# Kernel optimization log

Hardware: AMD Instinct MI355X
Metric: run time of the kernel (lower is better)

## Reference

```python
import jax, jax.numpy as jnp
import numpy as np
from jax import lax

RHO = 0.1          # init kwarg rho
CG_ITERS = 15      # dc_torch(..., 0.001, 15): fixed 15 CG iterations
EPS = 1e-12


def _c(x):  # (..., 2) real pair -> complex
    return lax.complex(x[..., 0], x[..., 1])


def _r(x):  # complex -> (..., 2) real pair
    return jnp.stack([jnp.real(x), jnp.imag(x)], axis=-1)


def fft2c(x):
    ax = (-2, -1)
    return jnp.fft.fftshift(jnp.fft.fft2(jnp.fft.ifftshift(x, axes=ax), axes=ax, norm='ortho'), axes=ax)


def ifft2c(x):
    ax = (-2, -1)
    return jnp.fft.fftshift(jnp.fft.ifft2(jnp.fft.ifftshift(x, axes=ax), axes=ax, norm='ortho'), axes=ax)


def setup_inputs() -> dict:
    key = jax.random.key(0)
    k0, k1, k2, k3 = jax.random.split(key, 4)
    B, S, C, H, W = 1, 4, 16, 320, 320
    K = jax.random.normal(k0, (B, S, C, H, W, 2), jnp.float32)
    I = jax.random.normal(k1, (B, S, H, W, 2), jnp.float32)
    csm = jax.random.normal(k2, (B, C, H, W, 2), jnp.float32) * 0.2
    mask = (jax.random.uniform(k3, (B, S, H, W)) < 0.35).astype(jnp.float32)
    return {'K_mulShot_sigCoil': K, 'I': I, 'csm': csm, 'mask': mask}


def _dc_cg(kdata, img, s, m):
    # kdata: [B,S,C,H,W] complex, img: [B,S,H,W], s: [B,C,H,W], m: [B,S,H,W]
    def E(x):                      # image [B,S,H,W] -> k-space [B,S,C,H,W]
        return m[:, :, None] * fft2c(s[:, None] * x[:, :, None])

    def EH(y):                     # adjoint: coil-combine
        return jnp.sum(jnp.conj(s)[:, None] * ifft2c(m[:, :, None] * y), axis=2)

    def AtA(x):
        return EH(E(x)) + RHO * x

    rhs = EH(kdata) + RHO * img
    x0 = jnp.zeros_like(rhs)
    r0 = rhs
    rs0 = jnp.real(jnp.vdot(r0, r0))

    def body(carry, _):
        x, r, p, rs = carry
        Ap = AtA(p)
        alpha = rs / (jnp.real(jnp.vdot(p, Ap)) + EPS)
        x = x + alpha * p
        r = r - alpha * Ap
        rs_new = jnp.real(jnp.vdot(r, r))
        p = r + (rs_new / (rs + EPS)) * p
        return (x, r, p, rs_new), None

    (x, _, _, _), _ = lax.scan(body, (x0, r0, r0, rs0), None, length=CG_ITERS)
    return x


def reference(K_mulShot_sigCoil, I, csm, mask):
    kdata = _c(K_mulShot_sigCoil)
    img = _c(I)
    s = _c(csm)
    x = _dc_cg(kdata, img, s, mask)   # image-domain CG solution
    K = fft2c(x)                      # sf.dc_torch returns k-space
    out = ifft2c(K)                   # layer returns I = ifft2c(K)
    return _r(out)
```

## Files before the change

### kernel.cpp

```cpp
#include <hip/hip_runtime.h>
#include <math.h>


#define NDIM 320
#define HHALF 160
#define HW (NDIM*NDIM)
#define NS 4
#define NC 16
#define RHO_ 0.1f
#define CG_ITERS 15

typedef float v2f __attribute__((ext_vector_type(2)));

__device__ __forceinline__ void wsync(){
    __builtin_amdgcn_fence(__ATOMIC_ACQ_REL, "wavefront");
    __builtin_amdgcn_wave_barrier();
}

__device__ __forceinline__ float wred(float v){
    #pragma unroll
    for (int o=32;o>0;o>>=1) v += __shfl_down(v,o,64);
    return v;
}

__device__ __forceinline__ v2f cmulf(v2f a, v2f b){
    return (v2f){a.x,a.x}*b + (v2f){-a.y,a.y}*(v2f){b.y,b.x};
}

template<int SIGMA>
__device__ __forceinline__ v2f cmulw(v2f a, v2f w){
    v2f wb = (SIGMA<0) ? w : (v2f){w.x, -w.y};
    return cmulf(a, wb);
}

template<int SIGMA>
__device__ __forceinline__ v2f mulj(v2f z){
    return (v2f){ -(float)SIGMA*z.y, (float)SIGMA*z.x };
}

template<int SIGMA>
__device__ __forceinline__ void radix5(const v2f* u, v2f* v){
    const float C1 = 0.30901699437494742f, S1 = 0.95105651629515357f;
    const float C2 = -0.80901699437494745f, S2 = 0.58778525229247312f;
    v2f t1=u[1]+u[4], t2=u[2]+u[3], t3=u[1]-u[4], t4=u[2]-u[3];
    v[0] = u[0] + t1 + t2;
    v2f m1 = u[0] + t1*C1 + t2*C2;
    v2f m2 = u[0] + t1*C2 + t2*C1;
    v2f n1 = t3*S1 + t4*S2;
    v2f n2 = t3*S2 - t4*S1;
    v2f j1 = mulj<SIGMA>(n1), j2 = mulj<SIGMA>(n2);
    v[1]=m1+j1; v[4]=m1-j1; v[2]=m2+j2; v[3]=m2-j2;
}

template<int SIGMA>
__device__ __forceinline__ void dft8(const v2f* u, v2f* y){
    const float C = 0.70710678118654752f;
    v2f a0=u[0]+u[4], a1=u[0]-u[4];
    v2f a2=u[2]+u[6], a3=u[2]-u[6];
    v2f a4=u[1]+u[5], a5=u[1]-u[5];
    v2f a6=u[3]+u[7], a7=u[3]-u[7];
    v2f j3 = mulj<SIGMA>(a3);
    v2f E0=a0+a2, E2=a0-a2;
    v2f E1=a1+j3, E3=a1-j3;
    v2f j7 = mulj<SIGMA>(a7);
    v2f O0=a4+a6, O2=a4-a6;
    v2f O1=a5+j7, O3=a5-j7;
    v2f W1 = (O1 + mulj<SIGMA>(O1)) * C;
    v2f jO2 = mulj<SIGMA>(O2);
    v2f W3 = (mulj<SIGMA>(O3) - O3) * C;
    y[0]=E0+O0; y[4]=E0-O0;
    y[1]=E1+W1; y[5]=E1-W1;
    y[2]=E2+jO2; y[6]=E2-jO2;
    y[3]=E3+W3; y[7]=E3-W3;
}

template<int SIGMA>
__device__ __forceinline__ void s1_from_regs(v2f* __restrict__ A, int t,
                                             const v2f* u5){
    v2f v[5];
    radix5<SIGMA>(u5, v);
    #pragma unroll
    for (int c=0;c<5;++c) A[5*t + c] = v[c];
}

template<int SIGMA>
__device__ __forceinline__ void s1_stage(v2f* __restrict__ A, int t){
    v2f u[5];
    #pragma unroll
    for (int q=0;q<5;++q) u[q] = A[t + 64*q];
    wsync();
    s1_from_regs<SIGMA>(A, t, u);
}

template<int SIGMA>
__device__ __forceinline__ void s2_stage(v2f* __restrict__ A, int t, v2f w40){
    if (t < 40){
        v2f u[8];
        #pragma unroll
        for (int q=0;q<8;++q) u[q] = A[t + 40*q];
        wsync();
        v2f wc = w40;
        u[1] = cmulw<SIGMA>(u[1], wc);
        #pragma unroll
        for (int q=2;q<8;++q){ wc = cmulf(wc, w40); u[q] = cmulw<SIGMA>(u[q], wc); }
        v2f v[8];
        dft8<SIGMA>(u, v);
        int k = t % 5, jb = t / 5;
        int base = jb*40 + k;
        #pragma unroll
        for (int c=0;c<8;++c) A[base + 5*c] = v[c];
    }
}

template<int SIGMA>
__device__ __forceinline__ void s3_toregs(const v2f* __restrict__ A, int t,
                                          v2f w320, v2f* v){
    if (t < 40){
        v2f u[8];
        #pragma unroll
        for (int q=0;q<8;++q) u[q] = A[t + 40*q];
        v2f wc = w320;
        u[1] = cmulw<SIGMA>(u[1], wc);
        #pragma unroll
        for (int q=2;q<8;++q){ wc = cmulf(wc, w320); u[q] = cmulw<SIGMA>(u[q], wc); }
        dft8<SIGMA>(u, v);
    }
}

template<int SIGMA>
__device__ __forceinline__ void a3_fromregs(v2f* __restrict__ A, int t,
                                            v2f w320, const v2f* vin){
    if (t < 40){
        v2f u[8];
        dft8<SIGMA>(vin, u);
        v2f wc = w320;
        u[1] = cmulw<SIGMA>(u[1], wc);
        #pragma unroll
        for (int q=2;q<8;++q){ wc = cmulf(wc, w320); u[q] = cmulw<SIGMA>(u[q], wc); }
        #pragma unroll
        for (int q=0;q<8;++q) A[t + 40*q] = u[q];
    }
}

template<int SIGMA>
__device__ __forceinline__ void a2_stage(v2f* __restrict__ A, int t, v2f w40){
    if (t < 40){
        int k = t % 5, jb = t / 5;
        int base = jb*40 + k;
        v2f v[8];
        #pragma unroll
        for (int c=0;c<8;++c) v[c] = A[base + 5*c];
        wsync();
        v2f u[8];
        dft8<SIGMA>(v, u);
        v2f wc = w40;
        u[1] = cmulw<SIGMA>(u[1], wc);
        #pragma unroll
        for (int q=2;q<8;++q){ wc = cmulf(wc, w40); u[q] = cmulw<SIGMA>(u[q], wc); }
        #pragma unroll
        for (int q=0;q<8;++q) A[t + 40*q] = u[q];
    }
}

template<int SIGMA>
__device__ __forceinline__ void a1_toregs(const v2f* __restrict__ A, int t,
                                          v2f* out5){
    v2f v[5];
    #pragma unroll
    for (int c=0;c<5;++c) v[c] = A[5*t + c];
    radix5<SIGMA>(v, out5);
}

__device__ __forceinline__ void make_w(int t, v2f& w40, v2f& w320){
    float sn, cs;
    const float n2pi = -6.283185307179586f;
    __sincosf(n2pi*(float)(t%5)/40.f, &sn, &cs); w40  = (v2f){cs, sn};
    __sincosf(n2pi*(float)t/320.f,    &sn, &cs); w320 = (v2f){cs, sn};
}

__device__ __forceinline__ int sh160(int i){ return i < HHALF ? i + HHALF : i - HHALF; }

__global__ void k_prep(const v2f* __restrict__ kin, const float* __restrict__ mask,
                       const v2f* __restrict__ csm, v2f* __restrict__ sP,
                       float* __restrict__ mscT, v2f* __restrict__ K,
                       float* __restrict__ scal)
{
    int gid = blockIdx.x*blockDim.x + threadIdx.x;
    int gsz = gridDim.x*blockDim.x;
    if (gid < 64) scal[gid] = 0.f;
    for (int i = gid; i < NC*HW; i += gsz){
        int w = i % NDIM; int h = (i/NDIM) % NDIM; int c = i/HW;
        sP[i] = csm[(c*NDIM + sh160(h))*NDIM + sh160(w)];
    }
    for (int i = gid; i < NS*HW; i += gsz){
        int h = i % NDIM; int wc = (i/NDIM)%NDIM; int s = i/HW;
        float m = mask[(s*NDIM + sh160(h))*NDIM + sh160(wc)];
        mscT[i] = m*m*(1.0f/102400.0f);
    }
    for (int i = gid; i < NS*NC*HW; i += gsz){
        int w = i % NDIM; int h = (i/NDIM)%NDIM; int sc = i/HW;
        int s = sc >> 4;
        int hs = sh160(h), ws = sh160(w);
        float m = mask[(s*NDIM + hs)*NDIM + ws];
        v2f kv = kin[((long)sc*NDIM + hs)*NDIM + ws];
        float f = m*(1.0f/320.0f);
        K[i] = kv * f;
    }
}

__global__ __launch_bounds__(256) void k_passA(
    const v2f* __restrict__ rv_, const v2f* __restrict__ pOld,
    v2f* __restrict__ pNew, const v2f* __restrict__ sP,
    v2f* __restrict__ K, float* __restrict__ scal, int iter)
{
    int bid = blockIdx.x;
    int cg = bid & 3;
    int hg = (bid>>2) % 80;
    int s  = bid / (4*80);
    int tid = threadIdx.x; int rl = tid>>6; int t = tid&63;
    int h = hg*4 + rl;
    __shared__ v2f bufA[4][NDIM];
    v2f* A = &bufA[rl][0];
    v2f w40, w320; make_w(t, w40, w320);
    float beta = 0.f;
    if (iter > 0) beta = scal[iter] / (scal[iter-1] + 1e-12f);
    long base = (long)s*HW + h*NDIM;
    v2f pv[5];
    #pragma unroll
    for (int j=0;j<5;++j){
        int idx = t + 64*j;
        v2f rr = rv_[base+idx];
        if (iter > 0){
            v2f pp = pOld[base+idx];
            pv[j] = rr + pp*beta;
        } else pv[j] = rr;
    }
    if (cg == 0){
        float d = 0.f;
        #pragma unroll
        for (int j=0;j<5;++j){
            pNew[base + t + 64*j] = pv[j];
            d += pv[j].x*pv[j].x + pv[j].y*pv[j].y;
        }
        float wd = wred(d);
        if (t==0) atomicAdd(&scal[16+iter], RHO_*wd);
    }
    int c = cg*4;
    const v2f* srow = sP + (long)c*HW + h*NDIM;
    v2f sv[5];
    #pragma unroll
    for (int j=0;j<5;++j) sv[j] = srow[t+64*j];
    #pragma unroll
    for (int c0=0;c0<4;++c0){
        v2f u5[5];
        #pragma unroll
        for (int j=0;j<5;++j) u5[j] = cmulf(sv[j], pv[j]);
        v2f sv2[5];
        if (c0<3){
            const v2f* sr2 = srow + (long)(c0+1)*HW;
            #pragma unroll
            for (int j=0;j<5;++j) sv2[j] = sr2[t+64*j];
        }
        wsync();
        s1_from_regs<-1>(A, t, u5);
        wsync();
        s2_stage<-1>(A, t, w40);
        wsync();
        v2f v8[8];
        s3_toregs<-1>(A, t, w320, v8);
        long kb = ((long)(s*NC + c + c0))*HW + h*NDIM;
        if (t < 40){
            #pragma unroll
            for (int cc=0;cc<8;++cc) K[kb + t + 40*cc] = v8[cc];
        }
        if (c0<3){
            #pragma unroll
            for (int j=0;j<5;++j) sv[j]=sv2[j];
        }
    }
}

__global__ __launch_bounds__(512) void k_passB(v2f* __restrict__ K,
    const float* __restrict__ mscT, int doMask)
{
    constexpr int L = 324;
    int bid = blockIdx.x;
    int wt = bid % 40;
    int sc = bid / 40;
    int s = sc >> 4;
    int tid = threadIdx.x;
    int col = tid >> 6;
    int t = tid & 63;
    int w0 = wt*8;
    __shared__ v2f bufA[8][L];
    v2f w40, w320; make_w(t, w40, w320);
    float mv[8];
    if (doMask && t < 40){
        const float* mcol = mscT + (long)s*HW + (long)(w0+col)*NDIM;
        #pragma unroll
        for (int cc=0;cc<8;++cc) mv[cc] = mcol[t+40*cc];
    }
    long gb = (long)sc*HW;
    int wl = tid & 7, hb = tid >> 3;
    #pragma unroll
    for (int j=0;j<5;++j){
        int hh = hb + 64*j;
        bufA[wl][hh] = K[gb + (long)hh*NDIM + w0 + wl];
    }
    __syncthreads();
    v2f* A = &bufA[col][0];
    if (doMask){
        s1_stage<-1>(A, t);
        wsync();
        s2_stage<-1>(A, t, w40);
        wsync();
        v2f v8[8];
        s3_toregs<-1>(A, t, w320, v8);
        if (t < 40){
            #pragma unroll
            for (int cc=0;cc<8;++cc) v8[cc] = v8[cc]*mv[cc];
        }
        wsync();
        a3_fromregs<1>(A, t, w320, v8);
        wsync();
        a2_stage<1>(A, t, w40);
        wsync();
        v2f x5[5];
        a1_toregs<1>(A, t, x5);
        wsync();
        #pragma unroll
        for (int q=0;q<5;++q) A[t + 64*q] = x5[q];
    } else {
        s1_stage<1>(A, t);
        wsync();
        s2_stage<1>(A, t, w40);
        wsync();
        v2f v8[8];
        s3_toregs<1>(A, t, w320, v8);
        wsync();
        if (t < 40){
            #pragma unroll
            for (int cc=0;cc<8;++cc) A[t + 40*cc] = v8[cc];
        }
    }
    __syncthreads();
    #pragma unroll
    for (int j=0;j<5;++j){
        int hh = hb + 64*j;
        K[gb + (long)hh*NDIM + w0 + wl] = bufA[wl][hh];
    }
}

__global__ __launch_bounds__(256) void k_passC2(
    const v2f* __restrict__ K, const v2f* __restrict__ sP,
    const v2f* __restrict__ pVec, v2f* __restrict__ part,
    float* __restrict__ scal, int dotSlot, int doDot)
{
    int bid = blockIdx.x;
    int cg = bid & 3;
    int hg = (bid>>2) % 80;
    int s  = bid / (4*80);
    int tid = threadIdx.x; int rl = tid>>6; int t = tid&63;
    int h = hg*4 + rl;
    __shared__ v2f bufA[4][NDIM];
    __shared__ float redS[4];
    v2f* A = &bufA[rl][0];
    v2f w40, w320; make_w(t, w40, w320);
    int c = cg*4;
    long kb0 = ((long)(s*NC + c))*HW + h*NDIM;
    const v2f* srow = sP + (long)c*HW + h*NDIM;
    v2f kv[8], sv[5];
    if (t < 40){
        #pragma unroll
        for (int cc=0;cc<8;++cc) kv[cc] = K[kb0 + t + 40*cc];
    }
    #pragma unroll
    for (int j=0;j<5;++j) sv[j] = srow[t+64*j];
    v2f acc[5];
    #pragma unroll
    for (int j=0;j<5;++j) acc[j]=(v2f){0.f,0.f};
    #pragma unroll
    for (int c0=0;c0<4;++c0){
        a3_fromregs<1>(A, t, w320, kv);
        v2f kv2[8], sv2[5];
        if (c0<3){
            long kb = kb0 + (long)(c0+1)*HW;
            const v2f* sr2 = srow + (long)(c0+1)*HW;
            if (t < 40){
                #pragma unroll
                for (int cc=0;cc<8;++cc) kv2[cc] = K[kb + t + 40*cc];
            }
            #pragma unroll
            for (int j=0;j<5;++j) sv2[j] = sr2[t+64*j];
        }
        wsync();
        a2_stage<1>(A, t, w40);
        wsync();
        v2f x5[5];
        a1_toregs<1>(A, t, x5);
        #pragma unroll
        for (int j=0;j<5;++j){
            acc[j] += (v2f){sv[j].x,sv[j].x}*x5[j]
                    + (v2f){sv[j].y,-sv[j].y}*(v2f){x5[j].y,x5[j].x};
        }
        wsync();
        if (c0<3){
            #pragma unroll
            for (int cc=0;cc<8;++cc) kv[cc]=kv2[cc];
            #pragma unroll
            for (int j=0;j<5;++j) sv[j]=sv2[j];
        }
    }
    long pbase = (long)s*HW + h*NDIM;
    long obase = ((long)cg*NS + s)*HW + h*NDIM;
    float dot = 0.f;
    #pragma unroll
    for (int j=0;j<5;++j){
        int idx=t+64*j;
        part[obase+idx] = acc[j];
        if (doDot){
            v2f pp = pVec[pbase+idx];
            dot += pp.x*acc[j].x + pp.y*acc[j].y;
        }
    }
    if (doDot){
        float wd = wred(dot);
        if (t==0) redS[rl] = wd;
        __syncthreads();
        if (tid==0) atomicAdd(&scal[dotSlot], redS[0]+redS[1]+redS[2]+redS[3]);
    }
}

__global__ __launch_bounds__(256) void k_rhs_fin(
    const v2f* __restrict__ part, const v2f* __restrict__ Iin,
    v2f* __restrict__ r, v2f* __restrict__ x, float* __restrict__ scal)
{
    __shared__ float red[256];
    int gid = blockIdx.x*blockDim.x + threadIdx.x;
    int gsz = gridDim.x*blockDim.x;
    float rs = 0.f;
    const int NV = NS*HW;
    for (int i = gid; i < NV; i += gsz){
        int w = i % NDIM; int h = (i/NDIM)%NDIM; int s = i/HW;
        v2f iv = Iin[((long)s*NDIM + sh160(h))*NDIM + sh160(w)];
        v2f rr = part[i] + part[NV+i] + part[2*NV+i] + part[3*NV+i] + iv*RHO_;
        r[i] = rr;
        x[i] = (v2f){0.f,0.f};
        rs += rr.x*rr.x + rr.y*rr.y;
    }
    red[threadIdx.x]=rs; __syncthreads();
    for (int o=128;o>0;o>>=1){ if (threadIdx.x<o) red[threadIdx.x]+=red[threadIdx.x+o]; __syncthreads(); }
    if (threadIdx.x==0) atomicAdd(&scal[0], red[0]);
}

__global__ __launch_bounds__(256) void k_update(
    v2f* __restrict__ x, v2f* __restrict__ r,
    const v2f* __restrict__ p, const v2f* __restrict__ part,
    float* __restrict__ scal, int iter)
{
    __shared__ float red[256];
    float alpha = scal[iter] / (scal[16+iter] + 1e-12f);
    int gid = blockIdx.x*blockDim.x + threadIdx.x;
    int gsz = gridDim.x*blockDim.x;
    float rs = 0.f;
    const int NV = NS*HW;
    for (int i = gid; i < NV; i += gsz){
        v2f pvv=p[i];
        v2f av = part[i] + part[NV+i] + part[2*NV+i] + part[3*NV+i] + pvv*RHO_;
        v2f xv = x[i] + pvv*alpha;
        v2f rv = r[i] - av*alpha;
        x[i]=xv; r[i]=rv;
        rs += rv.x*rv.x + rv.y*rv.y;
    }
    red[threadIdx.x]=rs; __syncthreads();
    for (int o=128;o>0;o>>=1){ if (threadIdx.x<o) red[threadIdx.x]+=red[threadIdx.x+o]; __syncthreads(); }
    if (threadIdx.x==0) atomicAdd(&scal[iter+1], red[0]);
}

__global__ void k_final(const v2f* __restrict__ x, v2f* __restrict__ out)
{
    int gid = blockIdx.x*blockDim.x + threadIdx.x;
    int gsz = gridDim.x*blockDim.x;
    for (int i = gid; i < NS*HW; i += gsz){
        int w = i % NDIM; int h = (i/NDIM)%NDIM; int s = i/HW;
        out[i] = x[(long)s*HW + sh160(h)*NDIM + sh160(w)];
    }
}

extern "C" void kernel_launch(void* const* d_in, const int* in_sizes, int n_in,
                              void* d_out, int out_size, void* d_ws, size_t ws_size,
                              hipStream_t stream) {
    (void)in_sizes; (void)n_in; (void)out_size; (void)ws_size;
    const v2f* kin  = (const v2f*)d_in[0];
    const v2f* Iin  = (const v2f*)d_in[1];
    const v2f* csm  = (const v2f*)d_in[2];
    const float* mask = (const float*)d_in[3];

    char* w = (char*)d_ws;
    size_t off = 0;
    float* scal = (float*)(w+off);  off += 1024;
    v2f* sP   = (v2f*)(w+off); off += (size_t)NC*HW*8;
    float* mscT = (float*)(w+off); off += (size_t)NS*HW*4;
    v2f* K    = (v2f*)(w+off); off += (size_t)NS*NC*HW*8;
    v2f* x    = (v2f*)(w+off); off += (size_t)NS*HW*8;
    v2f* r    = (v2f*)(w+off); off += (size_t)NS*HW*8;
    v2f* pA   = (v2f*)(w+off); off += (size_t)NS*HW*8;
    v2f* pB   = (v2f*)(w+off); off += (size_t)NS*HW*8;
    v2f* part = (v2f*)(w+off); off += (size_t)4*NS*HW*8;

    k_prep<<<2048,256,0,stream>>>(kin, mask, csm, sP, mscT, K, scal);
    k_passB<<<NS*NC*40,512,0,stream>>>(K, mscT, 0);
    k_passC2<<<NS*80*4,256,0,stream>>>(K, sP, r, part, scal, 63, 0);
    k_rhs_fin<<<640,256,0,stream>>>(part, Iin, r, x, scal);

    for (int it=0; it<CG_ITERS; ++it){
        v2f* pNew = (it&1)? pB : pA;
        v2f* pOld = (it&1)? pA : pB;
        k_passA<<<NS*80*4,256,0,stream>>>(r, pOld, pNew, sP, K, scal, it);
        k_passB<<<NS*NC*40,512,0,stream>>>(K, mscT, 1);
        k_passC2<<<NS*80*4,256,0,stream>>>(K, sP, pNew, part, scal, 16+it, 1);
        k_update<<<640,256,0,stream>>>(x, r, pNew, part, scal, it);
    }
    k_final<<<512,256,0,stream>>>(x, (v2f*)d_out);
}
```

Before: 1.617 ms.

## Process two FFT rows/columns per wavefront to raise per-thread ILP

Each 64-lane wavefront now computes two independent 320-point FFTs at once (paired radix-5/radix-8 stages) instead of one, in the row-forward, column, and adjoint-row kernels. The column kernel drops from 512 to 256 threads per block with the same eight columns per block, and the other kernels double shared memory per wave. The intent is to amortize twiddle generation, wave syncs and per-FFT overhead and to expose more instruction-level parallelism, at the cost of higher register pressure and fewer waves per block.

```diff
diff --git a/kernel.cpp b/kernel.cpp
--- a/kernel.cpp
+++ b/kernel.cpp
@@ -75,100 +75,123 @@
 }
 
 template<int SIGMA>
-__device__ __forceinline__ void s1_from_regs(v2f* __restrict__ A, int t,
-                                             const v2f* u5){
-    v2f v[5];
-    radix5<SIGMA>(u5, v);
-    #pragma unroll
-    for (int c=0;c<5;++c) A[5*t + c] = v[c];
-}
-
-template<int SIGMA>
-__device__ __forceinline__ void s1_stage(v2f* __restrict__ A, int t){
-    v2f u[5];
-    #pragma unroll
-    for (int q=0;q<5;++q) u[q] = A[t + 64*q];
+__device__ __forceinline__ void s1_write_pair(v2f* __restrict__ A0,
+                                              v2f* __restrict__ A1, int t,
+                                              const v2f* u0, const v2f* u1){
+    v2f v0[5], v1[5];
+    radix5<SIGMA>(u0, v0);
+    radix5<SIGMA>(u1, v1);
+    #pragma unroll
+    for (int c=0;c<5;++c){ A0[5*t+c]=v0[c]; A1[5*t+c]=v1[c]; }
+}
+
+template<int SIGMA>
+__device__ __forceinline__ void s1_pair(v2f* __restrict__ A0,
+                                        v2f* __restrict__ A1, int t){
+    v2f u0[5], u1[5];
+    #pragma unroll
+    for (int q=0;q<5;++q){ u0[q]=A0[t+64*q]; u1[q]=A1[t+64*q]; }
     wsync();
-    s1_from_regs<SIGMA>(A, t, u);
-}
-
-template<int SIGMA>
-__device__ __forceinline__ void s2_stage(v2f* __restrict__ A, int t, v2f w40){
+    s1_write_pair<SIGMA>(A0,A1,t,u0,u1);
+}
+
+template<int SIGMA>
+__device__ __forceinline__ void tw_dft8_pair(v2f* u0, v2f* u1, v2f w,
+                                             v2f* v0, v2f* v1){
+    v2f wc = w;
+    u0[1]=cmulw<SIGMA>(u0[1],wc); u1[1]=cmulw<SIGMA>(u1[1],wc);
+    #pragma unroll
+    for (int q=2;q<8;++q){
+        wc = cmulf(wc, w);
+        u0[q]=cmulw<SIGMA>(u0[q],wc); u1[q]=cmulw<SIGMA>(u1[q],wc);
+    }
+    dft8<SIGMA>(u0, v0);
+    dft8<SIGMA>(u1, v1);
+}
+
+template<int SIGMA>
+__device__ __forceinline__ void s2_pair(v2f* __restrict__ A0,
+                                        v2f* __restrict__ A1, int t, v2f w40){
     if (t < 40){
-        v2f u[8];
-        #pragma unroll
-        for (int q=0;q<8;++q) u[q] = A[t + 40*q];
-        wsync();
-        v2f wc = w40;
-        u[1] = cmulw<SIGMA>(u[1], wc);
-        #pragma unroll
-        for (int q=2;q<8;++q){ wc = cmulf(wc, w40); u[q] = cmulw<SIGMA>(u[q], wc); }
-        v2f v[8];
-        dft8<SIGMA>(u, v);
+        v2f u0[8], u1[8];
+        #pragma unroll
+        for (int q=0;q<8;++q){ u0[q]=A0[t+40*q]; u1[q]=A1[t+40*q]; }
+        wsync();
+        v2f v0[8], v1[8];
+        tw_dft8_pair<SIGMA>(u0,u1,w40,v0,v1);
         int k = t % 5, jb = t / 5;
         int base = jb*40 + k;
         #pragma unroll
-        for (int c=0;c<8;++c) A[base + 5*c] = v[c];
-    }
-}
-
-template<int SIGMA>
-__device__ __forceinline__ void s3_toregs(const v2f* __restrict__ A, int t,
-                                          v2f w320, v2f* v){
+        for (int c=0;c<8;++c){ A0[base+5*c]=v0[c]; A1[base+5*c]=v1[c]; }
+    }
+}
+
+template<int SIGMA>
+__device__ __forceinline__ void s3_pair(const v2f* __restrict__ A0,
+                                        const v2f* __restrict__ A1, int t,
+                                        v2f w320, v2f* v0, v2f* v1){
     if (t < 40){
-        v2f u[8];
-        #pragma unroll
-        for (int q=0;q<8;++q) u[q] = A[t + 40*q];
+        v2f u0[8], u1[8];
+        #pragma unroll
+        for (int q=0;q<8;++q){ u0[q]=A0[t+40*q]; u1[q]=A1[t+40*q]; }
+        tw_dft8_pair<SIGMA>(u0,u1,w320,v0,v1);
+    }
+}
+
+template<int SIGMA>
+__device__ __forceinline__ void a3_pair(v2f* __restrict__ A0,
+                                        v2f* __restrict__ A1, int t,
+                                        v2f w320, const v2f* i0, const v2f* i1){
+    if (t < 40){
+        v2f u0[8], u1[8];
+        dft8<SIGMA>(i0, u0);
+        dft8<SIGMA>(i1, u1);
         v2f wc = w320;
-        u[1] = cmulw<SIGMA>(u[1], wc);
-        #pragma unroll
-        for (int q=2;q<8;++q){ wc = cmulf(wc, w320); u[q] = cmulw<SIGMA>(u[q], wc); }
-        dft8<SIGMA>(u, v);
-    }
-}
-
-template<int SIGMA>
-__device__ __forceinline__ void a3_fromregs(v2f* __restrict__ A, int t,
-                                            v2f w320, const v2f* vin){
-    if (t < 40){
-        v2f u[8];
-        dft8<SIGMA>(vin, u);
-        v2f wc = w320;
-        u[1] = cmulw<SIGMA>(u[1], wc);
-        #pragma unroll
-        for (int q=2;q<8;++q){ wc = cmulf(wc, w320); u[q] = cmulw<SIGMA>(u[q], wc); }
-        #pragma unroll
-        for (int q=0;q<8;++q) A[t + 40*q] = u[q];
-    }
-}
-
-template<int SIGMA>
-__device__ __forceinline__ void a2_stage(v2f* __restrict__ A, int t, v2f w40){
+        u0[1]=cmulw<SIGMA>(u0[1],wc); u1[1]=cmulw<SIGMA>(u1[1],wc);
+        #pragma unroll
+        for (int q=2;q<8;++q){
+            wc = cmulf(wc, w320);
+            u0[q]=cmulw<SIGMA>(u0[q],wc); u1[q]=cmulw<SIGMA>(u1[q],wc);
+        }
+        #pragma unroll
+        for (int q=0;q<8;++q){ A0[t+40*q]=u0[q]; A1[t+40*q]=u1[q]; }
+    }
+}
+
+template<int SIGMA>
+__device__ __forceinline__ void a2_pair(v2f* __restrict__ A0,
+                                        v2f* __restrict__ A1, int t, v2f w40){
     if (t < 40){
         int k = t % 5, jb = t / 5;
         int base = jb*40 + k;
-        v2f v[8];
-        #pragma unroll
-        for (int c=0;c<8;++c) v[c] = A[base + 5*c];
-        wsync();
-        v2f u[8];
-        dft8<SIGMA>(v, u);
+        v2f v0[8], v1[8];
+        #pragma unroll
+        for (int c=0;c<8;++c){ v0[c]=A0[base+5*c]; v1[c]=A1[base+5*c]; }
+        wsync();
+        v2f u0[8], u1[8];
+        dft8<SIGMA>(v0, u0);
+        dft8<SIGMA>(v1, u1);
         v2f wc = w40;
-        u[1] = cmulw<SIGMA>(u[1], wc);
-        #pragma unroll
-        for (int q=2;q<8;++q){ wc = cmulf(wc, w40); u[q] = cmulw<SIGMA>(u[q], wc); }
-        #pragma unroll
-        for (int q=0;q<8;++q) A[t + 40*q] = u[q];
-    }
-}
-
-template<int SIGMA>
-__device__ __forceinline__ void a1_toregs(const v2f* __restrict__ A, int t,
-                                          v2f* out5){
-    v2f v[5];
-    #pragma unroll
-    for (int c=0;c<5;++c) v[c] = A[5*t + c];
-    radix5<SIGMA>(v, out5);
+        u0[1]=cmulw<SIGMA>(u0[1],wc); u1[1]=cmulw<SIGMA>(u1[1],wc);
+        #pragma unroll
+        for (int q=2;q<8;++q){
+            wc = cmulf(wc, w40);
+            u0[q]=cmulw<SIGMA>(u0[q],wc); u1[q]=cmulw<SIGMA>(u1[q],wc);
+        }
+        #pragma unroll
+        for (int q=0;q<8;++q){ A0[t+40*q]=u0[q]; A1[t+40*q]=u1[q]; }
+    }
+}
+
+template<int SIGMA>
+__device__ __forceinline__ void a1_pair(const v2f* __restrict__ A0,
+                                        const v2f* __restrict__ A1, int t,
+                                        v2f* o0, v2f* o1){
+    v2f v0[5], v1[5];
+    #pragma unroll
+    for (int c=0;c<5;++c){ v0[c]=A0[5*t+c]; v1[c]=A1[5*t+c]; }
+    radix5<SIGMA>(v0, o0);
+    radix5<SIGMA>(v1, o1);
 }
 
 __device__ __forceinline__ void make_w(int t, v2f& w40, v2f& w320){
@@ -219,8 +242,9 @@
     int s  = bid / (4*80);
     int tid = threadIdx.x; int rl = tid>>6; int t = tid&63;
     int h = hg*4 + rl;
-    __shared__ v2f bufA[4][NDIM];
-    v2f* A = &bufA[rl][0];
+    __shared__ v2f buf[8][NDIM];
+    v2f* A0 = &buf[2*rl][0];
+    v2f* A1 = &buf[2*rl+1][0];
     v2f w40, w320; make_w(t, w40, w320);
     float beta = 0.f;
     if (iter > 0) beta = scal[iter] / (scal[iter-1] + 1e-12f);
@@ -247,40 +271,43 @@
     }
     int c = cg*4;
     const v2f* srow = sP + (long)c*HW + h*NDIM;
-    v2f sv[5];
-    #pragma unroll
-    for (int j=0;j<5;++j) sv[j] = srow[t+64*j];
-    #pragma unroll
-    for (int c0=0;c0<4;++c0){
-        v2f u5[5];
-        #pragma unroll
-        for (int j=0;j<5;++j) u5[j] = cmulf(sv[j], pv[j]);
-        v2f sv2[5];
-        if (c0<3){
-            const v2f* sr2 = srow + (long)(c0+1)*HW;
-            #pragma unroll
-            for (int j=0;j<5;++j) sv2[j] = sr2[t+64*j];
-        }
-        wsync();
-        s1_from_regs<-1>(A, t, u5);
-        wsync();
-        s2_stage<-1>(A, t, w40);
-        wsync();
-        v2f v8[8];
-        s3_toregs<-1>(A, t, w320, v8);
-        long kb = ((long)(s*NC + c + c0))*HW + h*NDIM;
+    v2f sv0[5], sv1[5];
+    #pragma unroll
+    for (int j=0;j<5;++j){ sv0[j] = srow[t+64*j]; sv1[j] = srow[HW + t+64*j]; }
+    #pragma unroll
+    for (int pair=0;pair<2;++pair){
+        v2f u0[5], u1[5];
+        #pragma unroll
+        for (int j=0;j<5;++j){ u0[j]=cmulf(sv0[j],pv[j]); u1[j]=cmulf(sv1[j],pv[j]); }
+        v2f sn0[5], sn1[5];
+        if (pair==0){
+            const v2f* sr2 = srow + (long)2*HW;
+            #pragma unroll
+            for (int j=0;j<5;++j){ sn0[j]=sr2[t+64*j]; sn1[j]=sr2[HW + t+64*j]; }
+        }
+        wsync();
+        s1_write_pair<-1>(A0,A1,t,u0,u1);
+        wsync();
+        s2_pair<-1>(A0,A1,t,w40);
+        wsync();
+        v2f v0[8], v1[8];
+        s3_pair<-1>(A0,A1,t,w320,v0,v1);
+        long kb = ((long)(s*NC + c + 2*pair))*HW + h*NDIM;
         if (t < 40){
             #pragma unroll
-            for (int cc=0;cc<8;++cc) K[kb + t + 40*cc] = v8[cc];
-        }
-        if (c0<3){
-            #pragma unroll
-            for (int j=0;j<5;++j) sv[j]=sv2[j];
-        }
-    }
-}
-
-__global__ __launch_bounds__(512) void k_passB(v2f* __restrict__ K,
+            for (int cc=0;cc<8;++cc){
+                K[kb + t + 40*cc]      = v0[cc];
+                K[kb + HW + t + 40*cc] = v1[cc];
+            }
+        }
+        if (pair==0){
+            #pragma unroll
+            for (int j=0;j<5;++j){ sv0[j]=sn0[j]; sv1[j]=sn1[j]; }
+        }
+    }
+}
+
+__global__ __launch_bounds__(256) void k_passB(v2f* __restrict__ K,
     const float* __restrict__ mscT, int doMask)
 {
     constexpr int L = 324;
@@ -292,62 +319,63 @@
     int col = tid >> 6;
     int t = tid & 63;
     int w0 = wt*8;
-    __shared__ v2f bufA[8][L];
+    __shared__ v2f buf[8][L];
+    v2f* A0 = &buf[2*col][0];
+    v2f* A1 = &buf[2*col+1][0];
     v2f w40, w320; make_w(t, w40, w320);
-    float mv[8];
+    float mv0[8], mv1[8];
     if (doMask && t < 40){
-        const float* mcol = mscT + (long)s*HW + (long)(w0+col)*NDIM;
-        #pragma unroll
-        for (int cc=0;cc<8;++cc) mv[cc] = mcol[t+40*cc];
+        const float* mcol = mscT + (long)s*HW + (long)(w0+2*col)*NDIM;
+        #pragma unroll
+        for (int cc=0;cc<8;++cc){ mv0[cc]=mcol[t+40*cc]; mv1[cc]=mcol[NDIM + t+40*cc]; }
     }
     long gb = (long)sc*HW;
     int wl = tid & 7, hb = tid >> 3;
     #pragma unroll
-    for (int j=0;j<5;++j){
-        int hh = hb + 64*j;
-        bufA[wl][hh] = K[gb + (long)hh*NDIM + w0 + wl];
+    for (int j=0;j<10;++j){
+        int hh = hb + 32*j;
+        buf[wl][hh] = K[gb + (long)hh*NDIM + w0 + wl];
     }
     __syncthreads();
-    v2f* A = &bufA[col][0];
     if (doMask){
-        s1_stage<-1>(A, t);
-        wsync();
-        s2_stage<-1>(A, t, w40);
-        wsync();
-        v2f v8[8];
-        s3_toregs<-1>(A, t, w320, v8);
+        s1_pair<-1>(A0,A1,t);
+        wsync();
+        s2_pair<-1>(A0,A1,t,w40);
+        wsync();
+        v2f v0[8], v1[8];
+        s3_pair<-1>(A0,A1,t,w320,v0,v1);
         if (t < 40){
             #pragma unroll
-            for (int cc=0;cc<8;++cc) v8[cc] = v8[cc]*mv[cc];
-        }
-        wsync();
-        a3_fromregs<1>(A, t, w320, v8);
-        wsync();
-        a2_stage<1>(A, t, w40);
-        wsync();
-        v2f x5[5];
-        a1_toregs<1>(A, t, x5);
-        wsync();
-        #pragma unroll
-        for (int q=0;q<5;++q) A[t + 64*q] = x5[q];
+            for (int cc=0;cc<8;++cc){ v0[cc]=v0[cc]*mv0[cc]; v1[cc]=v1[cc]*mv1[cc]; }
+        }
+        wsync();
+        a3_pair<1>(A0,A1,t,w320,v0,v1);
+        wsync();
+        a2_pair<1>(A0,A1,t,w40);
+        wsync();
+        v2f x0[5], x1[5];
+        a1_pair<1>(A0,A1,t,x0,x1);
+        wsync();
+        #pragma unroll
+        for (int q=0;q<5;++q){ A0[t+64*q]=x0[q]; A1[t+64*q]=x1[q]; }
     } else {
-        s1_stage<1>(A, t);
-        wsync();
-        s2_stage<1>(A, t, w40);
-        wsync();
-        v2f v8[8];
-        s3_toregs<1>(A, t, w320, v8);
+        s1_pair<1>(A0,A1,t);
+        wsync();
+        s2_pair<1>(A0,A1,t,w40);
+        wsync();
+        v2f v0[8], v1[8];
+        s3_pair<1>(A0,A1,t,w320,v0,v1);
         wsync();
         if (t < 40){
             #pragma unroll
-            for (int cc=0;cc<8;++cc) A[t + 40*cc] = v8[cc];
+            for (int cc=0;cc<8;++cc){ A0[t+40*cc]=v0[cc]; A1[t+40*cc]=v1[cc]; }
         }
     }
     __syncthreads();
     #pragma unroll
-    for (int j=0;j<5;++j){
-        int hh = hb + 64*j;
-        K[gb + (long)hh*NDIM + w0 + wl] = bufA[wl][hh];
+    for (int j=0;j<10;++j){
+        int hh = hb + 32*j;
+        K[gb + (long)hh*NDIM + w0 + wl] = buf[wl][hh];
     }
 }
 
@@ -362,53 +390,56 @@
     int s  = bid / (4*80);
     int tid = threadIdx.x; int rl = tid>>6; int t = tid&63;
     int h = hg*4 + rl;
-    __shared__ v2f bufA[4][NDIM];
+    __shared__ v2f buf[8][NDIM];
     __shared__ float redS[4];
-    v2f* A = &bufA[rl][0];
+    v2f* A0 = &buf[2*rl][0];
+    v2f* A1 = &buf[2*rl+1][0];
     v2f w40, w320; make_w(t, w40, w320);
     int c = cg*4;
     long kb0 = ((long)(s*NC + c))*HW + h*NDIM;
     const v2f* srow = sP + (long)c*HW + h*NDIM;
-    v2f kv[8], sv[5];
+    v2f kv0[8], kv1[8], sv0[5], sv1[5];
     if (t < 40){
         #pragma unroll
-        for (int cc=0;cc<8;++cc) kv[cc] = K[kb0 + t + 40*cc];
-    }
-    #pragma unroll
-    for (int j=0;j<5;++j) sv[j] = srow[t+64*j];
+        for (int cc=0;cc<8;++cc){ kv0[cc]=K[kb0 + t+40*cc]; kv1[cc]=K[kb0 + HW + t+40*cc]; }
+    }
+    #pragma unroll
+    for (int j=0;j<5;++j){ sv0[j]=srow[t+64*j]; sv1[j]=srow[HW + t+64*j]; }
     v2f acc[5];
     #pragma unroll
     for (int j=0;j<5;++j) acc[j]=(v2f){0.f,0.f};
     #pragma unroll
-    for (int c0=0;c0<4;++c0){
-        a3_fromregs<1>(A, t, w320, kv);
-        v2f kv2[8], sv2[5];
-        if (c0<3){
-            long kb = kb0 + (long)(c0+1)*HW;
-            const v2f* sr2 = srow + (long)(c0+1)*HW;
+    for (int pair=0;pair<2;++pair){
+        a3_pair<1>(A0,A1,t,w320,kv0,kv1);
+        v2f kn0[8], kn1[8], sn0[5], sn1[5];
+        if (pair==0){
+            long kb = kb0 + (long)2*HW;
+            const v2f* sr2 = srow + (long)2*HW;
             if (t < 40){
                 #pragma unroll
-                for (int cc=0;cc<8;++cc) kv2[cc] = K[kb + t + 40*cc];
+                for (int cc=0;cc<8;++cc){ kn0[cc]=K[kb + t+40*cc]; kn1[cc]=K[kb + HW + t+40*cc]; }
             }
             #pragma unroll
-            for (int j=0;j<5;++j) sv2[j] = sr2[t+64*j];
-        }
-        wsync();
-        a2_stage<1>(A, t, w40);
-        wsync();
-        v2f x5[5];
-        a1_toregs<1>(A, t, x5);
+            for (int j=0;j<5;++j){ sn0[j]=sr2[t+64*j]; sn1[j]=sr2[HW + t+64*j]; }
+        }
+        wsync();
+        a2_pair<1>(A0,A1,t,w40);
+        wsync();
+        v2f x0[5], x1[5];
+        a1_pair<1>(A0,A1,t,x0,x1);
         #pragma unroll
         for (int j=0;j<5;++j){
-            acc[j] += (v2f){sv[j].x,sv[j].x}*x5[j]
-                    + (v2f){sv[j].y,-sv[j].y}*(v2f){x5[j].y,x5[j].x};
-        }
-        wsync();
-        if (c0<3){
-            #pragma unroll
-            for (int cc=0;cc<8;++cc) kv[cc]=kv2[cc];
-            #pragma unroll
-            for (int j=0;j<5;++j) sv[j]=sv2[j];
+            acc[j] += (v2f){sv0[j].x,sv0[j].x}*x0[j]
+                    + (v2f){sv0[j].y,-sv0[j].y}*(v2f){x0[j].y,x0[j].x};
+            acc[j] += (v2f){sv1[j].x,sv1[j].x}*x1[j]
+                    + (v2f){sv1[j].y,-sv1[j].y}*(v2f){x1[j].y,x1[j].x};
+        }
+        wsync();
+        if (pair==0){
+            #pragma unroll
+            for (int cc=0;cc<8;++cc){ kv0[cc]=kn0[cc]; kv1[cc]=kn1[cc]; }
+            #pragma unroll
+            for (int j=0;j<5;++j){ sv0[j]=sn0[j]; sv1[j]=sn1[j]; }
         }
     }
     long pbase = (long)s*HW + h*NDIM;
@@ -509,7 +540,7 @@
     v2f* part = (v2f*)(w+off); off += (size_t)4*NS*HW*8;
 
     k_prep<<<2048,256,0,stream>>>(kin, mask, csm, sP, mscT, K, scal);
-    k_passB<<<NS*NC*40,512,0,stream>>>(K, mscT, 0);
+    k_passB<<<NS*NC*40,256,0,stream>>>(K, mscT, 0);
     k_passC2<<<NS*80*4,256,0,stream>>>(K, sP, r, part, scal, 63, 0);
     k_rhs_fin<<<640,256,0,stream>>>(part, Iin, r, x, scal);
 
@@ -517,7 +548,7 @@
         v2f* pNew = (it&1)? pB : pA;
         v2f* pOld = (it&1)? pA : pB;
         k_passA<<<NS*80*4,256,0,stream>>>(r, pOld, pNew, sP, K, scal, it);
-        k_passB<<<NS*NC*40,512,0,stream>>>(K, mscT, 1);
+        k_passB<<<NS*NC*40,256,0,stream>>>(K, mscT, 1);
         k_passC2<<<NS*80*4,256,0,stream>>>(K, sP, pNew, part, scal, 16+it, 1);
         k_update<<<640,256,0,stream>>>(x, r, pNew, part, scal, it);
     }
```

Result: no change. 1.636 ms (+1.2%).
